# Kernel optimization log

Hardware: AMD Instinct MI355X
Metric: run time of the kernel (lower is better)

Reference implementation:

```python
import jax, jax.numpy as jnp
import numpy as np

B, P, S, D = 32, 16, 256, 256   # batch, pathways, substructures, embed dim
NG = 128                        # nodes per graph (fixed)
N = B * NG                      # total nodes
E = 65536                       # total edges
H = 256                         # hidden dim


def setup_inputs() -> dict:
    key = jax.random.key(0)
    ks = jax.random.split(key, 5)
    return {
        "drug_graph_embedding": jax.random.normal(ks[0], (B, P, S, D), jnp.float32),
        "global_ids": jax.random.randint(ks[1], (B, NG), 0, S),
        "edge_index": jax.random.randint(ks[2], (2, E), 0, N),
        "W1": jax.random.normal(ks[3], (D, H), jnp.float32) / np.sqrt(D).astype(np.float32),
        "b1": jnp.zeros((H,), jnp.float32),
        "W2": jax.random.normal(ks[4], (H, H), jnp.float32) / np.sqrt(H).astype(np.float32),
        "b2": jnp.zeros((H,), jnp.float32),
    }


def _gcn(x, W, b, src, dst, norm, n):
    # GCNConv: out[v] = sum_{u->v} norm(u,v) * (x[u] @ W) + b  (self-loops already in src/dst)
    h = x @ W
    msg = h[src] * norm[:, None]
    return jax.ops.segment_sum(msg, dst, num_segments=n) + b


def reference(drug_graph_embedding, global_ids, edge_index, W1, b1, W2, b2):
    b_, p_, s_, d_ = drug_graph_embedding.shape
    n = b_ * NG
    # mean over pathway axis -> [B, S, D]
    updated = drug_graph_embedding.mean(axis=1)
    # per-graph gather of substructure embeddings by global_ids -> [N, D]
    # (global_ids are generated < S, so the torch `if global_id < S` guard is always true)
    node_x = jax.vmap(lambda u, g: u[g])(updated, global_ids).reshape(n, d_)
    # add self-loops, symmetric GCN normalization D^{-1/2} (A+I) D^{-1/2}
    loops = jnp.arange(n)
    src = jnp.concatenate([edge_index[0], loops])
    dst = jnp.concatenate([edge_index[1], loops])
    deg = jax.ops.segment_sum(jnp.ones_like(dst, jnp.float32), dst, num_segments=n)
    dis = jax.lax.rsqrt(deg)  # deg >= 1 due to self-loops
    norm = dis[src] * dis[dst]
    x = _gcn(node_x, W1, b1, src, dst, norm, n)
    x = jax.nn.relu(x)
    x = _gcn(x, W2, b2, src, dst, norm, n)
    # global mean pool per graph (NG nodes each)
    batch = jnp.repeat(jnp.arange(b_), NG)
    return jax.ops.segment_sum(x, batch, num_segments=b_) / NG
```

## Files before the change

kernel.cpp:

```cpp
#include <hip/hip_runtime.h>
#include <hip/hip_bf16.h>

#define B_  32
#define P_  16
#define S_  256
#define D_  256
#define NG_ 128
#define N_  (B_ * NG_)
#define E_  65536
#define H_  256
#define CAP 128

__global__ __launch_bounds__(64) void k_node_mean(
    const float* __restrict__ emb, const int* __restrict__ gids,
    float* __restrict__ node_x) {
  const int n = blockIdx.x;
  const int b = n >> 7;
  const int g = n & (NG_ - 1);
  const int s = gids[b * NG_ + g];
  const int t = threadIdx.x;
  const float4* base = (const float4*)(emb + (size_t)b * (P_ * S_ * D_) + (size_t)s * D_) + t;
  float4 acc = {0.f, 0.f, 0.f, 0.f};
#pragma unroll
  for (int p = 0; p < P_; ++p) {
    float4 v = base[(size_t)p * (S_ * D_ / 4)];
    acc.x += v.x; acc.y += v.y; acc.z += v.z; acc.w += v.w;
  }
  const float inv = 1.0f / P_;
  acc.x *= inv; acc.y *= inv; acc.z *= inv; acc.w *= inv;
  ((float4*)(node_x + (size_t)n * D_))[t] = acc;
}

__global__ void k_zero(int* __restrict__ cnt) {
  int i = blockIdx.x * blockDim.x + threadIdx.x;
  if (i < N_) cnt[i] = 0;
}

__global__ void k_build(const int* __restrict__ src, const int* __restrict__ dst,
                        int* __restrict__ cnt, int* __restrict__ bucket) {
  int e = blockIdx.x * blockDim.x + threadIdx.x;
  if (e < E_) {
    int d = dst[e], s = src[e];
    int pos = atomicAdd(&cnt[d], 1);
    if (pos < CAP) bucket[(size_t)d * CAP + pos] = s;
  }
}

#define BM 32
#define BN 64
#define BK 32
#define LDA (BM + 2)
#define LDB (BN + 4)
__global__ __launch_bounds__(256) void k_gemm(
    const float* __restrict__ x, const float* __restrict__ W,
    float* __restrict__ out) {
  __shared__ float As[BK][LDA];
  __shared__ float Bs[BK][LDB];
  const int tid = threadIdx.x;
  const int m0 = (blockIdx.x >> 2) * BM;
  const int n0 = (blockIdx.x & 3) * BN;
  const int ar  = tid >> 3;
  const int ak  = (tid & 7) * 4;
  const int bkr = tid >> 4;
  const int bn  = (tid & 15) * 4;
  const int tx = tid & 15;
  const int ty = tid >> 4;

  float acc[2][4] = {};
  float4 a0 = *(const float4*)(x + (size_t)(m0 + ar) * D_ + ak);
  float4 b0 = *(const float4*)(W + (size_t)bkr * H_ + n0 + bn);
  float4 b1 = *(const float4*)(W + (size_t)(bkr + 16) * H_ + n0 + bn);

  for (int kk = 0; kk < D_; kk += BK) {
    __syncthreads();
    As[ak + 0][ar] = a0.x; As[ak + 1][ar] = a0.y;
    As[ak + 2][ar] = a0.z; As[ak + 3][ar] = a0.w;
    *(float4*)&Bs[bkr][bn] = b0;
    *(float4*)&Bs[bkr + 16][bn] = b1;
    __syncthreads();
    if (kk + BK < D_) {
      a0 = *(const float4*)(x + (size_t)(m0 + ar) * D_ + kk + BK + ak);
      b0 = *(const float4*)(W + (size_t)(kk + BK + bkr) * H_ + n0 + bn);
      b1 = *(const float4*)(W + (size_t)(kk + BK + bkr + 16) * H_ + n0 + bn);
    }
#pragma unroll
    for (int k = 0; k < BK; ++k) {
      const float2 a = *(const float2*)&As[k][ty * 2];
      const float4 b = *(const float4*)&Bs[k][tx * 4];
      acc[0][0] = fmaf(a.x, b.x, acc[0][0]); acc[0][1] = fmaf(a.x, b.y, acc[0][1]);
      acc[0][2] = fmaf(a.x, b.z, acc[0][2]); acc[0][3] = fmaf(a.x, b.w, acc[0][3]);
      acc[1][0] = fmaf(a.y, b.x, acc[1][0]); acc[1][1] = fmaf(a.y, b.y, acc[1][1]);
      acc[1][2] = fmaf(a.y, b.z, acc[1][2]); acc[1][3] = fmaf(a.y, b.w, acc[1][3]);
    }
  }
#pragma unroll
  for (int i = 0; i < 2; ++i) {
    float4 v = {acc[i][0], acc[i][1], acc[i][2], acc[i][3]};
    *(float4*)(out + (size_t)(m0 + ty * 2 + i) * H_ + n0 + tx * 4) = v;
  }
}

template <int RELU>
__global__ __launch_bounds__(256) void k_agg(
    const float* __restrict__ h, const float* __restrict__ bias,
    const int* __restrict__ cnt, const int* __restrict__ bucket,
    float* __restrict__ out) {
  __shared__ int   us[CAP];
  __shared__ float fs[CAP];
  const int v = blockIdx.x;
  const int t = threadIdx.x;
  const int deg = cnt[v];
  const float dv = rsqrtf(1.0f + (float)deg);
  const int m = deg > CAP ? CAP : deg;
  if (t < m) {
    const int u = bucket[(size_t)v * CAP + t];
    us[t] = u;
    fs[t] = dv * rsqrtf(1.0f + (float)cnt[u]);
  }
  __syncthreads();
  float acc = bias[t] + dv * dv * h[(size_t)v * H_ + t];
  int i = 0;
  for (; i + 4 <= m; i += 4) {
    const int u0 = us[i], u1 = us[i + 1], u2 = us[i + 2], u3 = us[i + 3];
    const float f0 = fs[i], f1 = fs[i + 1], f2 = fs[i + 2], f3 = fs[i + 3];
    const float h0 = h[(size_t)u0 * H_ + t];
    const float h1 = h[(size_t)u1 * H_ + t];
    const float h2 = h[(size_t)u2 * H_ + t];
    const float h3 = h[(size_t)u3 * H_ + t];
    acc = fmaf(f0, h0, acc); acc = fmaf(f1, h1, acc);
    acc = fmaf(f2, h2, acc); acc = fmaf(f3, h3, acc);
  }
  for (; i < m; ++i) acc = fmaf(fs[i], h[(size_t)us[i] * H_ + t], acc);
  if (RELU) acc = fmaxf(acc, 0.f);
  out[(size_t)v * H_ + t] = acc;
}

__global__ __launch_bounds__(256) void k_pool(
    const float* __restrict__ x2, float* __restrict__ out) {
  const int b = blockIdx.x;
  const int t = threadIdx.x;
  float acc = 0.f;
#pragma unroll 8
  for (int g = 0; g < NG_; ++g) acc += x2[(size_t)((b << 7) + g) * H_ + t];
  out[(size_t)b * H_ + t] = acc * (1.0f / NG_);
}

extern "C" void kernel_launch(void* const* d_in, const int* in_sizes, int n_in,
                              void* d_out, int out_size, void* d_ws, size_t ws_size,
                              hipStream_t stream) {
  const float* emb  = (const float*)d_in[0];
  const int*   gids = (const int*)d_in[1];
  const int*   eidx = (const int*)d_in[2];
  const float* W1   = (const float*)d_in[3];
  const float* b1   = (const float*)d_in[4];
  const float* W2   = (const float*)d_in[5];
  const float* b2   = (const float*)d_in[6];
  float* out = (float*)d_out;

  const int* src = eidx;
  const int* dst = eidx + E_;

  float* ws = (float*)d_ws;
  float* node_x = ws;
  float* hbuf   = node_x + (size_t)N_ * D_;
  float* x1     = hbuf   + (size_t)N_ * H_;
  float* x2     = x1     + (size_t)N_ * H_;
  int*   cnt    = (int*)(x2 + (size_t)N_ * H_);
  int*   bucket = cnt + N_;

  k_node_mean<<<N_, 64, 0, stream>>>(emb, gids, node_x);

  k_zero<<<(N_ + 255) / 256, 256, 0, stream>>>(cnt);
  k_build<<<(E_ + 255) / 256, 256, 0, stream>>>(src, dst, cnt, bucket);

  k_gemm<<<(N_ / BM) * (H_ / BN), 256, 0, stream>>>(node_x, W1, hbuf);
  k_agg<1><<<N_, 256, 0, stream>>>(hbuf, b1, cnt, bucket, x1);

  k_gemm<<<(N_ / BM) * (H_ / BN), 256, 0, stream>>>(x1, W2, hbuf);
  k_agg<0><<<N_, 256, 0, stream>>>(hbuf, b2, cnt, bucket, x2);

  k_pool<<<B_, 256, 0, stream>>>(x2, out);
}
```

Before: 247.6 us.

## Fold second GCN aggregation and mean pool into per-graph weighted node sum

```diff
diff --git a/kernel.cpp b/kernel.cpp
--- a/kernel.cpp
+++ b/kernel.cpp
@@ -9,16 +9,23 @@
 #define N_  (B_ * NG_)
 #define E_  65536
 #define H_  256
-#define CAP 128
+#define CAP 64
+#define BG  4
+#define UC  256
 
 __global__ __launch_bounds__(64) void k_node_mean(
     const float* __restrict__ emb, const int* __restrict__ gids,
-    float* __restrict__ node_x) {
+    float* __restrict__ node_x, int* __restrict__ cnt,
+    float* __restrict__ w2, float* __restrict__ outp) {
   const int n = blockIdx.x;
+  const int t = threadIdx.x;
+  if (t == 0) cnt[n] = 0;
+  const int gt = (n << 6) + t;
+  if (gt < B_ * N_) w2[gt] = 0.f;
+  if (gt < B_ * H_) outp[gt] = 0.f;
   const int b = n >> 7;
   const int g = n & (NG_ - 1);
   const int s = gids[b * NG_ + g];
-  const int t = threadIdx.x;
   const float4* base = (const float4*)(emb + (size_t)b * (P_ * S_ * D_) + (size_t)s * D_) + t;
   float4 acc = {0.f, 0.f, 0.f, 0.f};
 #pragma unroll
@@ -29,11 +36,6 @@
   const float inv = 1.0f / P_;
   acc.x *= inv; acc.y *= inv; acc.z *= inv; acc.w *= inv;
   ((float4*)(node_x + (size_t)n * D_))[t] = acc;
-}
-
-__global__ void k_zero(int* __restrict__ cnt) {
-  int i = blockIdx.x * blockDim.x + threadIdx.x;
-  if (i < N_) cnt[i] = 0;
 }
 
 __global__ void k_build(const int* __restrict__ src, const int* __restrict__ dst,
@@ -100,11 +102,10 @@
   }
 }
 
-template <int RELU>
 __global__ __launch_bounds__(256) void k_agg(
     const float* __restrict__ h, const float* __restrict__ bias,
     const int* __restrict__ cnt, const int* __restrict__ bucket,
-    float* __restrict__ out) {
+    float* __restrict__ out, float* __restrict__ w2) {
   __shared__ int   us[CAP];
   __shared__ float fs[CAP];
   const int v = blockIdx.x;
@@ -112,11 +113,15 @@
   const int deg = cnt[v];
   const float dv = rsqrtf(1.0f + (float)deg);
   const int m = deg > CAP ? CAP : deg;
+  const int bg = v >> 7;
   if (t < m) {
     const int u = bucket[(size_t)v * CAP + t];
+    const float f = dv * rsqrtf(1.0f + (float)cnt[u]);
     us[t] = u;
-    fs[t] = dv * rsqrtf(1.0f + (float)cnt[u]);
-  }
+    fs[t] = f;
+    atomicAdd(&w2[(size_t)bg * N_ + u], f);
+  }
+  if (t == 0) atomicAdd(&w2[(size_t)bg * N_ + v], dv * dv);
   __syncthreads();
   float acc = bias[t] + dv * dv * h[(size_t)v * H_ + t];
   int i = 0;
@@ -131,18 +136,34 @@
     acc = fmaf(f2, h2, acc); acc = fmaf(f3, h3, acc);
   }
   for (; i < m; ++i) acc = fmaf(fs[i], h[(size_t)us[i] * H_ + t], acc);
-  if (RELU) acc = fmaxf(acc, 0.f);
-  out[(size_t)v * H_ + t] = acc;
-}
-
-__global__ __launch_bounds__(256) void k_pool(
-    const float* __restrict__ x2, float* __restrict__ out) {
-  const int b = blockIdx.x;
+  out[(size_t)v * H_ + t] = fmaxf(acc, 0.f);
+}
+
+__global__ __launch_bounds__(256) void k_out(
+    const float* __restrict__ h2, const float* __restrict__ w2,
+    const float* __restrict__ b2, float* __restrict__ outp) {
+  __shared__ float wsh[BG][UC];
+  const int nuc = N_ / UC;
+  const int bg = blockIdx.x / nuc;
+  const int uc = blockIdx.x % nuc;
   const int t = threadIdx.x;
-  float acc = 0.f;
-#pragma unroll 8
-  for (int g = 0; g < NG_; ++g) acc += x2[(size_t)((b << 7) + g) * H_ + t];
-  out[(size_t)b * H_ + t] = acc * (1.0f / NG_);
+  const int u0 = uc * UC;
+#pragma unroll
+  for (int j = 0; j < BG; ++j)
+    wsh[j][t] = w2[(size_t)(bg * BG + j) * N_ + u0 + t];
+  __syncthreads();
+  float acc[BG] = {};
+#pragma unroll 4
+  for (int i = 0; i < UC; ++i) {
+    const float hv = h2[(size_t)(u0 + i) * H_ + t];
+#pragma unroll
+    for (int j = 0; j < BG; ++j) acc[j] = fmaf(wsh[j][i], hv, acc[j]);
+  }
+  const float inv = 1.0f / NG_;
+  const float bias = (uc == 0) ? b2[t] : 0.f;
+#pragma unroll
+  for (int j = 0; j < BG; ++j)
+    atomicAdd(&outp[(size_t)(bg * BG + j) * H_ + t], acc[j] * inv + bias);
 }
 
 extern "C" void kernel_launch(void* const* d_in, const int* in_sizes, int n_in,
@@ -164,20 +185,20 @@
   float* node_x = ws;
   float* hbuf   = node_x + (size_t)N_ * D_;
   float* x1     = hbuf   + (size_t)N_ * H_;
-  float* x2     = x1     + (size_t)N_ * H_;
-  int*   cnt    = (int*)(x2 + (size_t)N_ * H_);
+  float* h2     = x1     + (size_t)N_ * H_;
+  float* w2     = h2     + (size_t)N_ * H_;
+  int*   cnt    = (int*)(w2 + (size_t)B_ * N_);
   int*   bucket = cnt + N_;
 
-  k_node_mean<<<N_, 64, 0, stream>>>(emb, gids, node_x);
-
-  k_zero<<<(N_ + 255) / 256, 256, 0, stream>>>(cnt);
+  k_node_mean<<<N_, 64, 0, stream>>>(emb, gids, node_x, cnt, w2, out);
+
   k_build<<<(E_ + 255) / 256, 256, 0, stream>>>(src, dst, cnt, bucket);
 
   k_gemm<<<(N_ / BM) * (H_ / BN), 256, 0, stream>>>(node_x, W1, hbuf);
-  k_agg<1><<<N_, 256, 0, stream>>>(hbuf, b1, cnt, bucket, x1);
-
-  k_gemm<<<(N_ / BM) * (H_ / BN), 256, 0, stream>>>(x1, W2, hbuf);
-  k_agg<0><<<N_, 256, 0, stream>>>(hbuf, b2, cnt, bucket, x2);
-
-  k_pool<<<B_, 256, 0, stream>>>(x2, out);
-}
+
+  k_agg<<<N_, 256, 0, stream>>>(hbuf, b1, cnt, bucket, x1, w2);
+
+  k_gemm<<<(N_ / BM) * (H_ / BN), 256, 0, stream>>>(x1, W2, h2);
+
+  k_out<<<(B_ / BG) * (N_ / UC), 256, 0, stream>>>(h2, w2, b2, out);
+}
```

Result: no change. 247.4 us (-0.1%).
